# Optimization experiments

Hardware: AMD Instinct MI355X
Metric: run time of the kernel (lower is better)

## Reference

```python
import jax, jax.numpy as jnp
import numpy as np

# Transformer config constants (from init_kwargs)
SRF = 3.0                 # spatial_receptive_field
SRF2 = SRF * SRF
ALPHA = 2.0
BETA = 8.0
GAMMA = 16.0
RES = jnp.array([0.5, 0.5, 0.5], dtype=jnp.float32)   # relative_positional_gresolution
N_BUCKETS = 2 * 8 + 1                                  # 2*beta + 1 = 17
MUL = jnp.array([N_BUCKETS ** 2, N_BUCKETS, 1], dtype=jnp.float32)  # [289,17,1]
SLICES_PER_ROT = 2


def setup_inputs() -> dict:
    key = jax.random.key(0)
    k1, k2 = jax.random.split(key)
    N = 3072
    # LiDAR-like point coordinates in a 10m cube; receptive field 3.0 makes radius filter selective
    xyz = jax.random.uniform(k1, (N, 3), dtype=jnp.float32) * 10.0
    # grid columns: [batch, block, gx, gy, gz]; values < 128 per the torch assert
    grid = jax.random.randint(k2, (N, 5), 0, 8, dtype=jnp.int32)
    return {"xyz": xyz, "grid": grid}


def _bucket_base(x):
    # from_dxyz_to_bucket_base, res.size(0)==3 branch
    x = x / RES
    x_abs = jnp.abs(x)
    log_ratio = jnp.log(jnp.maximum(x_abs, 1e-6) / ALPHA) / np.log(GAMMA / ALPHA)
    sup = jnp.minimum(jnp.round(ALPHA - (BETA - ALPHA) * log_ratio), BETA)
    sup = jnp.sign(x) * sup
    return BETA + jnp.where(x_abs <= ALPHA, jnp.round(x), sup)


def reference(xyz, grid):
    # no-kvp path of jit_compute_interactions, expressed as dense [N,N] pair masks
    batch = grid[:, 0]
    block = grid[:, 1]
    coords = grid[:, 2:]            # grid_look[:, 1:]

    # batch equality filter (meshgrid + batch==batch)
    batch_eq = batch[:, None] == batch[None, :]
    # causal block filter: block[iq] <= block[ik]
    block_le = block[:, None] <= block[None, :]

    # force_keep_neighbours: adjacent voxels within the same block
    coord_adj = jnp.max(jnp.abs(coords[:, None, :] - coords[None, :, :]), axis=-1) <= 1
    forcekeep = coord_adj & (block[:, None] == block[None, :])

    # coarse spatial hash on xy: ceil(xy / srf), neighbor cells only
    xy_coarse = jnp.ceil(xyz[:, :2] / SRF).astype(jnp.int32)
    keep_coarse = jnp.max(jnp.abs(xy_coarse[:, None, :] - xy_coarse[None, :, :]), axis=-1) <= 1

    # pairwise deltas (torch uses fp16 here; fp32 kept for numerical clarity) [N,N,3]
    dxyz = xyz[:, None, :] - xyz[None, :, :]
    keepr = jnp.sum(dxyz * dxyz, axis=-1) <= SRF2

    mask = batch_eq & block_le & (forcekeep | keep_coarse) & (forcekeep | keepr)

    dxyz_m = jnp.where(mask[..., None], dxyz, 0.0)

    # from_dxyz_to_bucket_mul: log-bucketize each axis, flatten via mul_buckets
    buckets = jnp.sum(MUL * _bucket_base(dxyz_m), axis=-1).astype(jnp.int32)
    buckets = jnp.where(mask, buckets, 0)

    # dscanid = scanid[ik] - scanid[iq], scanid = block // slices_per_rotation
    scanid = block // SLICES_PER_ROT
    dscanid = jnp.where(mask, scanid[None, :] - scanid[:, None], 0)

    return dxyz_m, buckets, dscanid, mask
```

## Files before the change

### kernel.cpp

```cpp
#include <hip/hip_runtime.h>
#include <cmath>


__device__ __forceinline__ float bucket_base(float v) {
    const float x  = v * 2.0f;
    const float xa = fabsf(x);
    if (xa <= 2.0f) {
        return 8.0f + rintf(x);
    }
    const float lr = logf(fmaxf(xa, 1e-6f) * 0.5f) / 2.0794415416798357f;
    const float sup = fminf(rintf(2.0f - 6.0f * lr), 8.0f);
    return 8.0f + ((x > 0.0f) ? sup : -sup);
}

#define TPB 256
#define JB  1024

__global__ __launch_bounds__(256) void pair_kernel(
    const float* __restrict__ xyz, const int* __restrict__ grid,
    float* __restrict__ out, int N) {
#pragma clang fp contract(off)
    __shared__ float s_xyz[3 * JB];
    __shared__ int   s_grid[5 * JB];
    __shared__ float s_st[3 * JB];

    const int tid = threadIdx.x;
    const int i   = blockIdx.y;
    const int J0  = blockIdx.x * JB;

    {
        const float4* gx = reinterpret_cast<const float4*>(xyz + (size_t)3 * J0);
        float4* sx = reinterpret_cast<float4*>(s_xyz);
#pragma unroll
        for (int p = 0; p < 3; ++p) sx[TPB * p + tid] = gx[TPB * p + tid];
        const int4* gg = reinterpret_cast<const int4*>(grid + (size_t)5 * J0);
        int4* sg = reinterpret_cast<int4*>(s_grid);
#pragma unroll
        for (int p = 0; p < 5; ++p) sg[TPB * p + tid] = gg[TPB * p + tid];
    }

    const float xi = xyz[3 * i + 0];
    const float yi = xyz[3 * i + 1];
    const float zi = xyz[3 * i + 2];
    const int bat_i = grid[5 * i + 0];
    const int blk_i = grid[5 * i + 1];
    const int c0i = grid[5 * i + 2];
    const int c1i = grid[5 * i + 3];
    const int c2i = grid[5 * i + 4];
    const int xci = (int)ceilf(xi / 3.0f);
    const int yci = (int)ceilf(yi / 3.0f);
    const int scan_i = blk_i >> 1;

    __syncthreads();

    const int w   = tid >> 6;
    const int l   = tid & 63;
    const int jw0 = 256 * w;

    float dxm[4], dym[4], dzm[4];
    int   jblkA[4];
    bool  mk[4];
    bool  any = false;
#pragma unroll
    for (int k = 0; k < 4; ++k) {
        const int jl = jw0 + 64 * k + l;
        const float jx = s_xyz[3 * jl + 0];
        const float jy = s_xyz[3 * jl + 1];
        const float jz = s_xyz[3 * jl + 2];
        const int jbat = s_grid[5 * jl + 0];
        const int jblk = s_grid[5 * jl + 1];
        const int jc0  = s_grid[5 * jl + 2];
        const int jc1  = s_grid[5 * jl + 3];
        const int jc2  = s_grid[5 * jl + 4];

        const float dx = xi - jx;
        const float dy = yi - jy;
        const float dz = zi - jz;
        const bool batch_eq = (bat_i == jbat);
        const bool block_le = (blk_i <= jblk);
        const int  cadj = max(max(abs(c0i - jc0), abs(c1i - jc1)),
                              abs(c2i - jc2));
        const bool forcekeep = (cadj <= 1) && (blk_i == jblk);
        const int xcj = (int)ceilf(jx / 3.0f);
        const int ycj = (int)ceilf(jy / 3.0f);
        const bool keep_coarse = max(abs(xci - xcj), abs(yci - ycj)) <= 1;
        const float d2 = dx * dx + dy * dy + dz * dz;
        const bool keepr = (d2 <= 9.0f);
        const bool m = batch_eq && block_le &&
                       (forcekeep || keep_coarse) && (forcekeep || keepr);
        mk[k] = m;
        any |= m;
        jblkA[k] = jblk;
        dxm[k] = m ? dx : 0.0f;
        dym[k] = m ? dy : 0.0f;
        dzm[k] = m ? dz : 0.0f;
    }

    const size_t NN      = (size_t)N * (size_t)N;
    const size_t rowbase = (size_t)i * (size_t)N + (size_t)J0;
    float* __restrict__ obkt = out + NN * 3 + rowbase;
    float* __restrict__ odsc = out + NN * 4 + rowbase;
    float* __restrict__ omsk = out + NN * 5 + rowbase;
    float4* __restrict__ od4 =
        reinterpret_cast<float4*>(out + 3 * (rowbase + (size_t)jw0));

    if (__ballot(any ? 1 : 0) == 0ULL) {
        const float4 z4 = make_float4(0.0f, 0.0f, 0.0f, 0.0f);
#pragma unroll
        for (int p = 0; p < 3; ++p) od4[64 * p + l] = z4;
#pragma unroll
        for (int k = 0; k < 4; ++k) {
            const int jl = jw0 + 64 * k + l;
            obkt[jl] = 0.0f;
            odsc[jl] = 0.0f;
            omsk[jl] = 0.0f;
        }
        return;
    }

#pragma unroll
    for (int k = 0; k < 4; ++k) {
        const int jl = jw0 + 64 * k + l;
        float b = 0.0f, d = 0.0f, mvf = 0.0f;
        if (mk[k]) {
            const float b0 = bucket_base(dxm[k]);
            const float b1 = bucket_base(dym[k]);
            const float b2 = bucket_base(dzm[k]);
            const float bsum = (289.0f * b0 + 17.0f * b1) + b2;
            b   = (float)(int)bsum;
            d   = (float)((jblkA[k] >> 1) - scan_i);
            mvf = 1.0f;
        }
        obkt[jl] = b;
        odsc[jl] = d;
        omsk[jl] = mvf;
        s_st[3 * jl + 0] = dxm[k];
        s_st[3 * jl + 1] = dym[k];
        s_st[3 * jl + 2] = dzm[k];
    }

    const float4* st4 = reinterpret_cast<const float4*>(s_st + 3 * jw0);
#pragma unroll
    for (int p = 0; p < 3; ++p) od4[64 * p + l] = st4[64 * p + l];
}

extern "C" void kernel_launch(void* const* d_in, const int* in_sizes, int n_in,
                              void* d_out, int out_size, void* d_ws, size_t ws_size,
                              hipStream_t stream) {
    const float* xyz  = (const float*)d_in[0];
    const int*   grid = (const int*)d_in[1];
    float*       out  = (float*)d_out;
    const int N = in_sizes[0] / 3;

    dim3 gdim(N / JB, N, 1);
    pair_kernel<<<gdim, dim3(TPB, 1, 1), 0, stream>>>(xyz, grid, out, N);
}
```

Baseline: 215.9 us.

## Process multiple query rows per block with register-resident keys and nontemporal stores

```diff
diff --git a/kernel.cpp b/kernel.cpp
--- a/kernel.cpp
+++ b/kernel.cpp
@@ -1,6 +1,12 @@
 #include <hip/hip_runtime.h>
 #include <cmath>
 
+
+#define TPB 256
+#define JB  1024
+#define II  6
+
+typedef float f32x4 __attribute__((ext_vector_type(4)));
 
 __device__ __forceinline__ float bucket_base(float v) {
     const float x  = v * 2.0f;
@@ -13,135 +19,127 @@
     return 8.0f + ((x > 0.0f) ? sup : -sup);
 }
 
-#define TPB 256
-#define JB  1024
-
 __global__ __launch_bounds__(256) void pair_kernel(
     const float* __restrict__ xyz, const int* __restrict__ grid,
     float* __restrict__ out, int N) {
 #pragma clang fp contract(off)
-    __shared__ float s_xyz[3 * JB];
-    __shared__ int   s_grid[5 * JB];
     __shared__ float s_st[3 * JB];
 
     const int tid = threadIdx.x;
-    const int i   = blockIdx.y;
-    const int J0  = blockIdx.x * JB;
-
-    {
-        const float4* gx = reinterpret_cast<const float4*>(xyz + (size_t)3 * J0);
-        float4* sx = reinterpret_cast<float4*>(s_xyz);
-#pragma unroll
-        for (int p = 0; p < 3; ++p) sx[TPB * p + tid] = gx[TPB * p + tid];
-        const int4* gg = reinterpret_cast<const int4*>(grid + (size_t)5 * J0);
-        int4* sg = reinterpret_cast<int4*>(s_grid);
-#pragma unroll
-        for (int p = 0; p < 5; ++p) sg[TPB * p + tid] = gg[TPB * p + tid];
-    }
-
-    const float xi = xyz[3 * i + 0];
-    const float yi = xyz[3 * i + 1];
-    const float zi = xyz[3 * i + 2];
-    const int bat_i = grid[5 * i + 0];
-    const int blk_i = grid[5 * i + 1];
-    const int c0i = grid[5 * i + 2];
-    const int c1i = grid[5 * i + 3];
-    const int c2i = grid[5 * i + 4];
-    const int xci = (int)ceilf(xi / 3.0f);
-    const int yci = (int)ceilf(yi / 3.0f);
-    const int scan_i = blk_i >> 1;
-
-    __syncthreads();
-
     const int w   = tid >> 6;
     const int l   = tid & 63;
     const int jw0 = 256 * w;
+    const int J0  = blockIdx.x * JB;
+    const int I0  = blockIdx.y * II;
 
-    float dxm[4], dym[4], dzm[4];
-    int   jblkA[4];
-    bool  mk[4];
-    bool  any = false;
+    float jx[4], jy[4], jz[4];
+    int   jbat[4], jblk[4], jc0[4], jc1[4], jc2[4], xcj[4], ycj[4];
 #pragma unroll
     for (int k = 0; k < 4; ++k) {
-        const int jl = jw0 + 64 * k + l;
-        const float jx = s_xyz[3 * jl + 0];
-        const float jy = s_xyz[3 * jl + 1];
-        const float jz = s_xyz[3 * jl + 2];
-        const int jbat = s_grid[5 * jl + 0];
-        const int jblk = s_grid[5 * jl + 1];
-        const int jc0  = s_grid[5 * jl + 2];
-        const int jc1  = s_grid[5 * jl + 3];
-        const int jc2  = s_grid[5 * jl + 4];
-
-        const float dx = xi - jx;
-        const float dy = yi - jy;
-        const float dz = zi - jz;
-        const bool batch_eq = (bat_i == jbat);
-        const bool block_le = (blk_i <= jblk);
-        const int  cadj = max(max(abs(c0i - jc0), abs(c1i - jc1)),
-                              abs(c2i - jc2));
-        const bool forcekeep = (cadj <= 1) && (blk_i == jblk);
-        const int xcj = (int)ceilf(jx / 3.0f);
-        const int ycj = (int)ceilf(jy / 3.0f);
-        const bool keep_coarse = max(abs(xci - xcj), abs(yci - ycj)) <= 1;
-        const float d2 = dx * dx + dy * dy + dz * dz;
-        const bool keepr = (d2 <= 9.0f);
-        const bool m = batch_eq && block_le &&
-                       (forcekeep || keep_coarse) && (forcekeep || keepr);
-        mk[k] = m;
-        any |= m;
-        jblkA[k] = jblk;
-        dxm[k] = m ? dx : 0.0f;
-        dym[k] = m ? dy : 0.0f;
-        dzm[k] = m ? dz : 0.0f;
+        const int j = J0 + jw0 + 64 * k + l;
+        jx[k]   = xyz[3 * j + 0];
+        jy[k]   = xyz[3 * j + 1];
+        jz[k]   = xyz[3 * j + 2];
+        jbat[k] = grid[5 * j + 0];
+        jblk[k] = grid[5 * j + 1];
+        jc0[k]  = grid[5 * j + 2];
+        jc1[k]  = grid[5 * j + 3];
+        jc2[k]  = grid[5 * j + 4];
+        xcj[k] = (int)ceilf(jx[k] / 3.0f);
+        ycj[k] = (int)ceilf(jy[k] / 3.0f);
     }
 
-    const size_t NN      = (size_t)N * (size_t)N;
-    const size_t rowbase = (size_t)i * (size_t)N + (size_t)J0;
-    float* __restrict__ obkt = out + NN * 3 + rowbase;
-    float* __restrict__ odsc = out + NN * 4 + rowbase;
-    float* __restrict__ omsk = out + NN * 5 + rowbase;
-    float4* __restrict__ od4 =
-        reinterpret_cast<float4*>(out + 3 * (rowbase + (size_t)jw0));
+    const size_t NN = (size_t)N * (size_t)N;
 
-    if (__ballot(any ? 1 : 0) == 0ULL) {
-        const float4 z4 = make_float4(0.0f, 0.0f, 0.0f, 0.0f);
+    for (int ii = 0; ii < II; ++ii) {
+        const int i = I0 + ii;
+        if (i >= N) break;
+
+        const float xi = xyz[3 * i + 0];
+        const float yi = xyz[3 * i + 1];
+        const float zi = xyz[3 * i + 2];
+        const int bat_i = grid[5 * i + 0];
+        const int blk_i = grid[5 * i + 1];
+        const int c0i = grid[5 * i + 2];
+        const int c1i = grid[5 * i + 3];
+        const int c2i = grid[5 * i + 4];
+        const int xci = (int)ceilf(xi / 3.0f);
+        const int yci = (int)ceilf(yi / 3.0f);
+        const int scan_i = blk_i >> 1;
+
+        float dxm[4], dym[4], dzm[4];
+        bool  mk[4];
+        bool  any = false;
 #pragma unroll
-        for (int p = 0; p < 3; ++p) od4[64 * p + l] = z4;
+        for (int k = 0; k < 4; ++k) {
+            const float dx = xi - jx[k];
+            const float dy = yi - jy[k];
+            const float dz = zi - jz[k];
+            const bool batch_eq = (bat_i == jbat[k]);
+            const bool block_le = (blk_i <= jblk[k]);
+            const int  cadj = max(max(abs(c0i - jc0[k]), abs(c1i - jc1[k])),
+                                  abs(c2i - jc2[k]));
+            const bool forcekeep = (cadj <= 1) && (blk_i == jblk[k]);
+            const bool keep_coarse =
+                max(abs(xci - xcj[k]), abs(yci - ycj[k])) <= 1;
+            const float d2 = dx * dx + dy * dy + dz * dz;
+            const bool keepr = (d2 <= 9.0f);
+            const bool m = batch_eq && block_le &&
+                           (forcekeep || keep_coarse) && (forcekeep || keepr);
+            mk[k] = m;
+            any |= m;
+            dxm[k] = m ? dx : 0.0f;
+            dym[k] = m ? dy : 0.0f;
+            dzm[k] = m ? dz : 0.0f;
+        }
+
+        const size_t rowbase = (size_t)i * (size_t)N + (size_t)J0;
+        float* __restrict__ obkt = out + NN * 3 + rowbase;
+        float* __restrict__ odsc = out + NN * 4 + rowbase;
+        float* __restrict__ omsk = out + NN * 5 + rowbase;
+        f32x4* __restrict__ od4 =
+            reinterpret_cast<f32x4*>(out + 3 * (rowbase + (size_t)jw0));
+        f32x4* __restrict__ ob4 = reinterpret_cast<f32x4*>(obkt + jw0);
+        f32x4* __restrict__ os4 = reinterpret_cast<f32x4*>(odsc + jw0);
+        f32x4* __restrict__ om4 = reinterpret_cast<f32x4*>(omsk + jw0);
+
+        if (__ballot(any ? 1 : 0) == 0ULL) {
+            const f32x4 z4 = {0.0f, 0.0f, 0.0f, 0.0f};
+#pragma unroll
+            for (int p = 0; p < 3; ++p)
+                __builtin_nontemporal_store(z4, od4 + 64 * p + l);
+            __builtin_nontemporal_store(z4, ob4 + l);
+            __builtin_nontemporal_store(z4, os4 + l);
+            __builtin_nontemporal_store(z4, om4 + l);
+            continue;
+        }
+
 #pragma unroll
         for (int k = 0; k < 4; ++k) {
             const int jl = jw0 + 64 * k + l;
-            obkt[jl] = 0.0f;
-            odsc[jl] = 0.0f;
-            omsk[jl] = 0.0f;
+            float b = 0.0f, d = 0.0f, mvf = 0.0f;
+            if (mk[k]) {
+                const float b0 = bucket_base(dxm[k]);
+                const float b1 = bucket_base(dym[k]);
+                const float b2 = bucket_base(dzm[k]);
+                const float bsum = (289.0f * b0 + 17.0f * b1) + b2;
+                b   = (float)(int)bsum;
+                d   = (float)((jblk[k] >> 1) - scan_i);
+                mvf = 1.0f;
+            }
+            __builtin_nontemporal_store(b,   obkt + jl);
+            __builtin_nontemporal_store(d,   odsc + jl);
+            __builtin_nontemporal_store(mvf, omsk + jl);
+            s_st[3 * jl + 0] = dxm[k];
+            s_st[3 * jl + 1] = dym[k];
+            s_st[3 * jl + 2] = dzm[k];
         }
-        return;
+
+        const f32x4* st4 = reinterpret_cast<const f32x4*>(s_st + 3 * jw0);
+#pragma unroll
+        for (int p = 0; p < 3; ++p)
+            __builtin_nontemporal_store(st4[64 * p + l], od4 + 64 * p + l);
     }
-
-#pragma unroll
-    for (int k = 0; k < 4; ++k) {
-        const int jl = jw0 + 64 * k + l;
-        float b = 0.0f, d = 0.0f, mvf = 0.0f;
-        if (mk[k]) {
-            const float b0 = bucket_base(dxm[k]);
-            const float b1 = bucket_base(dym[k]);
-            const float b2 = bucket_base(dzm[k]);
-            const float bsum = (289.0f * b0 + 17.0f * b1) + b2;
-            b   = (float)(int)bsum;
-            d   = (float)((jblkA[k] >> 1) - scan_i);
-            mvf = 1.0f;
-        }
-        obkt[jl] = b;
-        odsc[jl] = d;
-        omsk[jl] = mvf;
-        s_st[3 * jl + 0] = dxm[k];
-        s_st[3 * jl + 1] = dym[k];
-        s_st[3 * jl + 2] = dzm[k];
-    }
-
-    const float4* st4 = reinterpret_cast<const float4*>(s_st + 3 * jw0);
-#pragma unroll
-    for (int p = 0; p < 3; ++p) od4[64 * p + l] = st4[64 * p + l];
 }
 
 extern "C" void kernel_launch(void* const* d_in, const int* in_sizes, int n_in,
@@ -152,6 +150,6 @@
     float*       out  = (float*)d_out;
     const int N = in_sizes[0] / 3;
 
-    dim3 gdim(N / JB, N, 1);
+    dim3 gdim(N / JB, (N + II - 1) / II, 1);
     pair_kernel<<<gdim, dim3(TPB, 1, 1), 0, stream>>>(xyz, grid, out, N);
 }
```

Measured after the change: 232.7 us. 7.8% more time.
